# Optimization experiments

Hardware: AMD Instinct MI355X
Metric: run time of the kernel (lower is better)

Reference implementation:

```python
import jax, jax.numpy as jnp
import numpy as np

B, N, DIM, H, DH = 2, 2048, 1024, 16, 64
ALPHA = 32.0 ** 2  # stable_softmax alpha
SCALE = DH ** -0.5


def rotate_half(x):
    # interleaved pairs: (x0, x1, x2, x3, ...) -> (-x1, x0, -x3, x2, ...)
    xp = x.reshape(x.shape[:-1] + (-1, 2))
    return jnp.stack((-xp[..., 1], xp[..., 0]), axis=-1).reshape(x.shape)


def apply_rotary(freqs, t):
    # freqs: [n, d]; t: [b, h, n, d]
    return t * jnp.cos(freqs) + rotate_half(t) * jnp.sin(freqs)


def setup_inputs() -> dict:
    key = jax.random.key(0)
    k0, k1, k2, k3 = jax.random.split(key, 4)
    x = jax.random.normal(k0, (B, N, DIM), jnp.float32)
    rotary_pos_emb = jax.random.normal(k1, (N, DH), jnp.float32)
    w_qkv = jax.random.normal(k2, (DIM, 3 * H * DH), jnp.float32) / np.sqrt(DIM)
    w_out = jax.random.normal(k3, (H * DH, DIM), jnp.float32) / np.sqrt(H * DH)
    b_out = jnp.zeros((DIM,), jnp.float32)
    return {"x": x, "rotary_pos_emb": rotary_pos_emb, "w_qkv": w_qkv,
            "w_out": w_out, "b_out": b_out}


def reference(x, rotary_pos_emb, w_qkv, w_out, b_out):
    b, n, _ = x.shape
    qkv = x @ w_qkv                                  # [b, n, 3*h*d]
    q, k, v = jnp.split(qkv, 3, axis=-1)
    to_heads = lambda t: t.reshape(b, n, H, DH).transpose(0, 2, 1, 3)  # [b,h,n,d]
    q, k, v = map(to_heads, (q, k, v))
    freqs = rotary_pos_emb[:n]
    # source applies rotary emb to q, k AND v
    q = apply_rotary(freqs, q)
    k = apply_rotary(freqs, k)
    v = apply_rotary(freqs, v)
    q = q * SCALE
    dots = jnp.einsum('bhid,bhjd->bhij', q, k)       # [b,h,n,n]
    mask_value = -jnp.finfo(dots.dtype).max
    causal = jnp.triu(jnp.ones((n, n), bool), 1)
    dots = jnp.where(causal, mask_value, dots)
    # stable softmax: divide by alpha, subtract detached max, rescale
    t = dots / ALPHA
    t = t - jax.lax.stop_gradient(jnp.max(t, axis=-1, keepdims=True))
    attn = jax.nn.softmax(t * ALPHA, axis=-1)
    out = jnp.einsum('bhij,bhjd->bhid', attn, v)     # [b,h,n,d]
    out = out.transpose(0, 2, 1, 3).reshape(b, n, H * DH)
    return out @ w_out + b_out
```

## Files before the change

### kernel.cpp

```cpp
#include <hip/hip_runtime.h>
#include <stdint.h>

#define DEV __device__ __forceinline__

typedef __bf16 bf16x8 __attribute__((ext_vector_type(8)));
typedef float  f32x4  __attribute__((ext_vector_type(4)));
typedef short  s16x8  __attribute__((ext_vector_type(8)));

constexpr int Bb   = 2;
constexpr int Nn   = 2048;
constexpr int DIMc = 1024;
constexpr int Hh   = 16;
constexpr int DHc  = 64;
constexpr int BN   = Bb * Nn;
constexpr int QKVC = 3 * Hh * DHc;

DEV ushort f2b(float f) {
  uint32_t u = __float_as_uint(f);
  u += 0x7fffu + ((u >> 16) & 1u);
  return (ushort)(u >> 16);
}

DEV void gload16(const void* g, void* l) {
  __builtin_amdgcn_global_load_lds(
      (const __attribute__((address_space(1))) void*)(uintptr_t)g,
      (__attribute__((address_space(3))) void*)(uint32_t)(uintptr_t)l,
      16, 0, 0);
}

DEV f32x4 mfma16(bf16x8 a, bf16x8 b, f32x4 c) {
  return __builtin_amdgcn_mfma_f32_16x16x32_bf16(a, b, c, 0, 0, 0);
}

DEV uint32_t cvtpk(float lo, float hi) {
  uint32_t r;
  asm("v_cvt_pk_bf16_f32 %0, %1, %2" : "=v"(r) : "v"(lo), "v"(hi));
  return r;
}


__global__ void k_cast_x(const float* __restrict__ x, ushort* __restrict__ xb) {
  int i = blockIdx.x * 256 + threadIdx.x;
  size_t base = (size_t)i * 8;
  s16x8 v;
#pragma unroll
  for (int j = 0; j < 8; ++j) v[j] = (short)f2b(x[base + j]);
  *(s16x8*)(xb + base) = v;
}

__global__ void k_sincos(const float* __restrict__ rope, float2* __restrict__ csT) {
  int i = blockIdx.x * 256 + threadIdx.x;
  float t = rope[i];
  float s, c;
  sincosf(t, &s, &c);
  csT[i] = make_float2(c, s);
}

__global__ void k_transpose_cast(const float* __restrict__ src, ushort* __restrict__ dst,
                                 int K, int Ncols) {
  __shared__ float tile[32][33];
  int nb = blockIdx.x * 32, kb = blockIdx.y * 32;
  int tx = threadIdx.x, ty = threadIdx.y;
#pragma unroll
  for (int i = 0; i < 4; ++i) {
    int k = ty + i * 8;
    tile[k][tx] = src[(size_t)(kb + k) * Ncols + nb + tx];
  }
  __syncthreads();
#pragma unroll
  for (int i = 0; i < 4; ++i) {
    int n = ty + i * 8;
    dst[(size_t)(nb + n) * K + kb + tx] = f2b(tile[tx][n]);
  }
}

DEV void gemm_core(const ushort* __restrict__ A, const ushort* __restrict__ Bt,
                   int rowBase, int colBase, ushort* lA, ushort* lB,
                   f32x4 (&acc)[4][4]) {
  const int tid = threadIdx.x;
  const int lane = tid & 63, w = tid >> 6;
  const int wm = w >> 1, wn = w & 1;
  const int g = lane >> 4, l16 = lane & 15;
  const f32x4 zero = {0.f, 0.f, 0.f, 0.f};
#pragma unroll
  for (int i = 0; i < 4; ++i)
#pragma unroll
    for (int j = 0; j < 4; ++j) acc[i][j] = zero;

  const int c0row = tid >> 2,          c0kc = (tid & 3) ^ ((c0row >> 1) & 3);
  const int c1row = (256 + tid) >> 2,  c1kc = (tid & 3) ^ ((c1row >> 1) & 3);
  const ushort* gA0 = A  + (size_t)(rowBase + c0row) * DIMc + c0kc * 8;
  const ushort* gA1 = A  + (size_t)(rowBase + c1row) * DIMc + c1kc * 8;
  const ushort* gB0 = Bt + (size_t)(colBase + c0row) * DIMc + c0kc * 8;
  const ushort* gB1 = Bt + (size_t)(colBase + c1row) * DIMc + c1kc * 8;
  const size_t o0 = (size_t)(0 * 256 + w * 64) * 8;
  const size_t o1 = (size_t)(1 * 256 + w * 64) * 8;
  constexpr int BUF = 128 * 32;

  gload16(gA0,      lA + o0);        gload16(gB0,      lB + o0);
  gload16(gA1,      lA + o1);        gload16(gB1,      lB + o1);
  gload16(gA0 + 32, lA + BUF + o0);  gload16(gB0 + 32, lB + BUF + o0);
  gload16(gA1 + 32, lA + BUF + o1);  gload16(gB1 + 32, lB + BUF + o1);
  asm volatile("s_waitcnt vmcnt(4)" ::: "memory");
  __builtin_amdgcn_s_barrier();

  int cur = 0;
  for (int k0 = 0; k0 < DIMc; k0 += 32) {
    const ushort* cA = lA + cur * BUF;
    const ushort* cB = lB + cur * BUF;

    bf16x8 af[4], bfr[4];
#pragma unroll
    for (int f = 0; f < 4; ++f) {
      int r  = wm * 64 + f * 16 + l16;
      int r2 = wn * 64 + f * 16 + l16;
      af[f]  = *(const bf16x8*)&cA[r  * 32 + ((g ^ ((r  >> 1) & 3)) << 3)];
      bfr[f] = *(const bf16x8*)&cB[r2 * 32 + ((g ^ ((r2 >> 1) & 3)) << 3)];
    }

    const int kn = k0 + 64;
    if (kn < DIMc) {
      int st = cur + 2; if (st >= 3) st -= 3;
      ushort* nA = lA + st * BUF;
      ushort* nB = lB + st * BUF;
      gload16(gA0 + kn, nA + o0);  gload16(gB0 + kn, nB + o0);
      gload16(gA1 + kn, nA + o1);  gload16(gB1 + kn, nB + o1);
    }

#pragma unroll
    for (int i = 0; i < 4; ++i)
#pragma unroll
      for (int j = 0; j < 4; ++j)
        acc[i][j] = mfma16(af[i], bfr[j], acc[i][j]);

    if (kn < DIMc) {
      asm volatile("s_waitcnt vmcnt(4)" ::: "memory");
    } else if (k0 + 32 < DIMc) {
      asm volatile("s_waitcnt vmcnt(0)" ::: "memory");
    }
    asm volatile("s_waitcnt lgkmcnt(0)" ::: "memory");
    __builtin_amdgcn_s_barrier();
    cur += 1; if (cur == 3) cur = 0;
  }
}

__global__ __launch_bounds__(256) void k_gemm_qkv(
    const ushort* __restrict__ xb, const ushort* __restrict__ wT,
    const float2* __restrict__ csT,
    ushort* __restrict__ Qd, ushort* __restrict__ Kd, ushort* __restrict__ Vd) {
  __shared__ ushort lA[3 * 128 * 32];
  __shared__ ushort lB[3 * 128 * 32];
  f32x4 acc[4][4];
  const int rowBase = blockIdx.y * 128, colBase = blockIdx.x * 128;
  gemm_core(xb, wT, rowBase, colBase, lA, lB, acc);

  const int lane = threadIdx.x & 63, w = threadIdx.x >> 6;
  const int wm = w >> 1, wn = w & 1;
  const int g = lane >> 4, l16 = lane & 15;
#pragma unroll
  for (int fm = 0; fm < 4; ++fm) {
#pragma unroll
    for (int fn = 0; fn < 4; ++fn) {
      int col = colBase + wn * 64 + fn * 16 + l16;
      int sel = col >> 10, hc = col & 1023;
      int h = hc >> 6, d = hc & 63;
      float sgn = (d & 1) ? 1.f : -1.f;
#pragma unroll
      for (int r = 0; r < 4; ++r) {
        float t  = acc[fm][fn][r];
        float tp = __shfl_xor(t, 1);
        int row = rowBase + wm * 64 + fm * 16 + 4 * g + r;
        int b = row >> 11, n = row & 2047;
        float2 cs = csT[n * 64 + d];
        float rv = t * cs.x + sgn * tp * cs.y;
        if (sel == 0) {
          Qd[((size_t)(b * Hh + h) * Nn + n) * DHc + d] = f2b(rv * 0.125f);
        } else if (sel == 1) {
          Kd[((size_t)(b * Hh + h) * Nn + n) * DHc + d] = f2b(rv);
        } else {
          Vd[((size_t)(b * Hh + h) * DHc + d) * Nn + n] = f2b(rv);
        }
      }
    }
  }
}


DEV void stageKV(const ushort* __restrict__ Kh, const ushort* __restrict__ Vh,
                 ushort* lKb, ushort* lVb, int kt, int tid, int w) {
#pragma unroll
  for (int s = 0; s < 2; ++s) {
    int c = s * 256 + tid;
    int row = c >> 3, jst = c & 7;
    int jl = jst ^ (row & 7);
    gload16(Kh + (size_t)(kt * 64 + row) * DHc + jl * 8,
            lKb + (size_t)(s * 256 + w * 64) * 8);
    gload16(Vh + (size_t)row * Nn + kt * 64 + jl * 8,
            lVb + (size_t)(s * 256 + w * 64) * 8);
  }
}

DEV void attn_step(const ushort* lKc, const ushort* lVc, char* lPw,
                   const bf16x8 (&q)[2], f32x4 (&o)[4], float& m, float& l,
                   int kBase, int qg, bool diag, int g, int l16) {
  const f32x4 zero = {0.f, 0.f, 0.f, 0.f};
  f32x4 s[4];
#pragma unroll
  for (int jt = 0; jt < 4; ++jt) s[jt] = zero;

#pragma unroll
  for (int jt = 0; jt < 4; ++jt) {
    int jr = jt * 16 + l16;
#pragma unroll
    for (int d0 = 0; d0 < 2; ++d0) {
      bf16x8 kb = *(const bf16x8*)&lKc[jr * 64 + (((d0 * 4 + g) ^ (jr & 7)) << 3)];
      s[jt] = mfma16(kb, q[d0], s[jt]);
    }
  }

  if (diag) {
#pragma unroll
    for (int jt = 0; jt < 4; ++jt)
#pragma unroll
      for (int r = 0; r < 4; ++r) {
        int j = kBase + jt * 16 + 4 * g + r;
        if (j > qg) s[jt][r] = -3.0e38f;
      }
  }

  float tmax = fmaxf(fmaxf(fmaxf(s[0][0], s[0][1]), fmaxf(s[0][2], s[0][3])),
                     fmaxf(fmaxf(s[1][0], s[1][1]), fmaxf(s[1][2], s[1][3])));
  tmax = fmaxf(tmax, fmaxf(fmaxf(fmaxf(s[2][0], s[2][1]), fmaxf(s[2][2], s[2][3])),
                           fmaxf(fmaxf(s[3][0], s[3][1]), fmaxf(s[3][2], s[3][3]))));
  tmax = fmaxf(tmax, __shfl_xor(tmax, 16));
  tmax = fmaxf(tmax, __shfl_xor(tmax, 32));

  if (!__all(tmax <= m + 8.f)) {
    float mnew = fmaxf(m, tmax);
    float sc = __expf(m - mnew);
#pragma unroll
    for (int dt = 0; dt < 4; ++dt) o[dt] *= sc;
    l *= sc;
    m = mnew;
  }

  float ps = 0.f;
#pragma unroll
  for (int jt = 0; jt < 4; ++jt)
#pragma unroll
    for (int r = 0; r < 4; ++r) {
      float p = __expf(s[jt][r] - m);
      s[jt][r] = p;
      ps += p;
    }
  ps += __shfl_xor(ps, 16);
  ps += __shfl_xor(ps, 32);
  l += ps;

  const int sw = (l16 & 7) << 4;
  char* prow = lPw + l16 * 128;
#pragma unroll
  for (int jt = 0; jt < 4; ++jt) {
    int jo = (jt * 16 + 4 * g) * 2;
    *(uint32_t*)(prow + (jo ^ sw))       = cvtpk(s[jt][0], s[jt][1]);
    *(uint32_t*)(prow + ((jo + 4) ^ sw)) = cvtpk(s[jt][2], s[jt][3]);
  }

  bf16x8 pa[2];
#pragma unroll
  for (int jh = 0; jh < 2; ++jh)
    pa[jh] = *(const bf16x8*)(prow + (((jh * 32 + 8 * g) * 2) ^ sw));
#pragma unroll
  for (int dt = 0; dt < 4; ++dt) {
    int d = dt * 16 + l16;
#pragma unroll
    for (int jh = 0; jh < 2; ++jh) {
      bf16x8 vb = *(const bf16x8*)&lVc[d * 64 + (((jh * 4 + g) ^ (d & 7)) << 3)];
      o[dt] = mfma16(vb, pa[jh], o[dt]);
    }
  }
}

DEV void attn_epi(ushort* __restrict__ ao, int bh, int n, int g,
                  f32x4 (&o)[4], float l) {
  const int b = bh >> 4, h = bh & 15;
  float inv = 1.f / l;
  ushort* dst = ao + (size_t)(b * Nn + n) * (Hh * DHc) + h * 64;
#pragma unroll
  for (int dt = 0; dt < 4; ++dt) {
    uint2 pkd;
    pkd.x = cvtpk(o[dt][0] * inv, o[dt][1] * inv);
    pkd.y = cvtpk(o[dt][2] * inv, o[dt][3] * inv);
    *(uint2*)(dst + dt * 16 + 4 * g) = pkd;
  }
}

__global__ __launch_bounds__(256) void k_attn(
    const ushort* __restrict__ Qd, const ushort* __restrict__ Kd,
    const ushort* __restrict__ Vd, ushort* __restrict__ ao) {
  __shared__ ushort lK[2][64 * 64];
  __shared__ ushort lV[2][64 * 64];
  __shared__ char   lP[4][16 * 128];
  const int tid = threadIdx.x;
  const int lane = tid & 63, w = tid >> 6;
  const int g = lane >> 4, l16 = lane & 15;
  const int bh = blockIdx.y;
  const int p = blockIdx.x;
  const int tA = p, tB = 31 - p;
  const int last = tB;
  const ushort* Qh = Qd + (size_t)bh * Nn * DHc;
  const ushort* Kh = Kd + (size_t)bh * Nn * DHc;
  const ushort* Vh = Vd + (size_t)bh * DHc * Nn;

  const int qgA = tA * 64 + w * 16 + l16;
  const int qgB = tB * 64 + w * 16 + l16;

  bf16x8 qA[2], qB[2];
#pragma unroll
  for (int d0 = 0; d0 < 2; ++d0) {
    qA[d0] = *(const bf16x8*)(Qh + (size_t)qgA * DHc + d0 * 32 + g * 8);
    qB[d0] = *(const bf16x8*)(Qh + (size_t)qgB * DHc + d0 * 32 + g * 8);
  }

  const f32x4 zero = {0.f, 0.f, 0.f, 0.f};
  f32x4 oA[4], oB[4];
#pragma unroll
  for (int dt = 0; dt < 4; ++dt) { oA[dt] = zero; oB[dt] = zero; }
  float mA = -3.0e38f, lA_ = 0.f, mB = -3.0e38f, lB_ = 0.f;

  stageKV(Kh, Vh, lK[0], lV[0], 0, tid, w);

  for (int kt = 0; kt <= last; ++kt) {
    const int cur = kt & 1;
    if (kt < last) {
      stageKV(Kh, Vh, lK[cur ^ 1], lV[cur ^ 1], kt + 1, tid, w);
      asm volatile("s_waitcnt vmcnt(4)" ::: "memory");
    } else {
      asm volatile("s_waitcnt vmcnt(0)" ::: "memory");
    }
    __builtin_amdgcn_s_barrier();

    attn_step(lK[cur], lV[cur], lP[w], qB, oB, mB, lB_, kt * 64, qgB, kt == tB, g, l16);
    if (kt <= tA)
      attn_step(lK[cur], lV[cur], lP[w], qA, oA, mA, lA_, kt * 64, qgA, kt == tA, g, l16);

    __builtin_amdgcn_s_barrier();
  }

  attn_epi(ao, bh, qgA, g, oA, lA_);
  attn_epi(ao, bh, qgB, g, oB, lB_);
}

__global__ __launch_bounds__(256) void k_gemm_out(
    const ushort* __restrict__ ao, const ushort* __restrict__ wT,
    const float* __restrict__ bias, float* __restrict__ out) {
  __shared__ ushort lA[3 * 128 * 32];
  __shared__ ushort lB[3 * 128 * 32];
  f32x4 acc[4][4];
  const int rowBase = blockIdx.y * 128, colBase = blockIdx.x * 128;
  gemm_core(ao, wT, rowBase, colBase, lA, lB, acc);

  const int lane = threadIdx.x & 63, w = threadIdx.x >> 6;
  const int wm = w >> 1, wn = w & 1;
  const int g = lane >> 4, l16 = lane & 15;
#pragma unroll
  for (int fm = 0; fm < 4; ++fm)
#pragma unroll
    for (int fn = 0; fn < 4; ++fn) {
      int col = colBase + wn * 64 + fn * 16 + l16;
#pragma unroll
      for (int r = 0; r < 4; ++r) {
        int row = rowBase + wm * 64 + fm * 16 + 4 * g + r;
        out[(size_t)row * DIMc + col] = acc[fm][fn][r] + bias[col];
      }
    }
}

extern "C" void kernel_launch(void* const* d_in, const int* in_sizes, int n_in,
                              void* d_out, int out_size, void* d_ws, size_t ws_size,
                              hipStream_t stream) {
  const float* x     = (const float*)d_in[0];
  const float* rope  = (const float*)d_in[1];
  const float* w_qkv = (const float*)d_in[2];
  const float* w_out = (const float*)d_in[3];
  const float* b_out = (const float*)d_in[4];
  float* out = (float*)d_out;

  char* ws = (char*)d_ws;
  ushort* xb    = (ushort*)(ws);
  ushort* wqkvT = (ushort*)(ws + 8388608);
  ushort* woutT = (ushort*)(ws + 14680064);
  float2* csT   = (float2*)(ws + 16777216);
  ushort* Qd    = (ushort*)(ws + 17825792);
  ushort* Kd    = (ushort*)(ws + 26214400);
  ushort* Vd    = (ushort*)(ws + 34603008);
  ushort* ao    = (ushort*)(ws + 42991616);

  hipLaunchKernelGGL(k_cast_x, dim3(2048), dim3(256), 0, stream, x, xb);
  hipLaunchKernelGGL(k_transpose_cast, dim3(QKVC / 32, DIMc / 32), dim3(32, 8), 0, stream,
                     w_qkv, wqkvT, DIMc, QKVC);
  hipLaunchKernelGGL(k_transpose_cast, dim3(DIMc / 32, DIMc / 32), dim3(32, 8), 0, stream,
                     w_out, woutT, DIMc, DIMc);
  hipLaunchKernelGGL(k_sincos, dim3(Nn * DHc / 256), dim3(256), 0, stream, rope, csT);
  hipLaunchKernelGGL(k_gemm_qkv, dim3(QKVC / 128, BN / 128), dim3(256), 0, stream,
                     xb, wqkvT, csT, Qd, Kd, Vd);
  hipLaunchKernelGGL(k_attn, dim3(16, Bb * Hh), dim3(256), 0, stream, Qd, Kd, Vd, ao);
  hipLaunchKernelGGL(k_gemm_out, dim3(DIMc / 128, BN / 128), dim3(256), 0, stream,
                     ao, woutT, b_out, out);
}
```

Before: 131.1 us.

## Fuse sincos into cast kernel and shrink out-projection GEMM tile to 64x128

Folds the rotary sin/cos precompute into the x cast kernel, removing one launch. Rewrites the output projection GEMM with its own 64x128 tile loop, a triple-buffered LDS pipeline and four waves each owning a 32-column strip. This doubles the block count from 256 to 512 to fill more CUs on the 4096x1024 output, at the cost of less data reuse per block.

```diff
diff --git a/kernel.cpp b/kernel.cpp
--- a/kernel.cpp
+++ b/kernel.cpp
@@ -39,21 +39,20 @@
 }
 
 
-__global__ void k_cast_x(const float* __restrict__ x, ushort* __restrict__ xb) {
+__global__ void k_cast_x(const float* __restrict__ x, ushort* __restrict__ xb,
+                         const float* __restrict__ rope, float2* __restrict__ csT) {
   int i = blockIdx.x * 256 + threadIdx.x;
   size_t base = (size_t)i * 8;
   s16x8 v;
 #pragma unroll
   for (int j = 0; j < 8; ++j) v[j] = (short)f2b(x[base + j]);
   *(s16x8*)(xb + base) = v;
-}
-
-__global__ void k_sincos(const float* __restrict__ rope, float2* __restrict__ csT) {
-  int i = blockIdx.x * 256 + threadIdx.x;
-  float t = rope[i];
-  float s, c;
-  sincosf(t, &s, &c);
-  csT[i] = make_float2(c, s);
+  if (i < Nn * DHc) {
+    float t = rope[i];
+    float s, c;
+    sincosf(t, &s, &c);
+    csT[i] = make_float2(c, s);
+  }
 }
 
 __global__ void k_transpose_cast(const float* __restrict__ src, ushort* __restrict__ dst,
@@ -354,23 +353,82 @@
 __global__ __launch_bounds__(256) void k_gemm_out(
     const ushort* __restrict__ ao, const ushort* __restrict__ wT,
     const float* __restrict__ bias, float* __restrict__ out) {
-  __shared__ ushort lA[3 * 128 * 32];
+  __shared__ ushort lA[3 * 64 * 32];
   __shared__ ushort lB[3 * 128 * 32];
-  f32x4 acc[4][4];
-  const int rowBase = blockIdx.y * 128, colBase = blockIdx.x * 128;
-  gemm_core(ao, wT, rowBase, colBase, lA, lB, acc);
-
-  const int lane = threadIdx.x & 63, w = threadIdx.x >> 6;
-  const int wm = w >> 1, wn = w & 1;
+  const int tid = threadIdx.x;
+  const int lane = tid & 63, w = tid >> 6;
   const int g = lane >> 4, l16 = lane & 15;
+  const int rowBase = blockIdx.y * 64, colBase = blockIdx.x * 128;
+
+  f32x4 acc[4][2];
+  const f32x4 zero = {0.f, 0.f, 0.f, 0.f};
+#pragma unroll
+  for (int i = 0; i < 4; ++i) { acc[i][0] = zero; acc[i][1] = zero; }
+
+  const int arow = tid >> 2, akc = (tid & 3) ^ ((arow >> 1) & 3);
+  const int b1row = 64 + arow, b1kc = (tid & 3) ^ ((b1row >> 1) & 3);
+  const ushort* gA  = ao + (size_t)(rowBase + arow) * DIMc + akc * 8;
+  const ushort* gB0 = wT + (size_t)(colBase + arow) * DIMc + akc * 8;
+  const ushort* gB1 = wT + (size_t)(colBase + b1row) * DIMc + b1kc * 8;
+  const size_t oA  = (size_t)w * 512;
+  const size_t oB0 = (size_t)w * 512;
+  const size_t oB1 = 2048 + (size_t)w * 512;
+  constexpr int BUFA = 64 * 32, BUFB = 128 * 32;
+
+  gload16(gA,      lA + oA);         gload16(gB0,      lB + oB0);         gload16(gB1,      lB + oB1);
+  gload16(gA + 32, lA + BUFA + oA);  gload16(gB0 + 32, lB + BUFB + oB0);  gload16(gB1 + 32, lB + BUFB + oB1);
+  asm volatile("s_waitcnt vmcnt(3)" ::: "memory");
+  __builtin_amdgcn_s_barrier();
+
+  int cur = 0;
+  for (int k0 = 0; k0 < DIMc; k0 += 32) {
+    const ushort* cA = lA + cur * BUFA;
+    const ushort* cB = lB + cur * BUFB;
+
+    bf16x8 af[4], bfr[2];
+#pragma unroll
+    for (int f = 0; f < 4; ++f) {
+      int r = f * 16 + l16;
+      af[f] = *(const bf16x8*)&cA[r * 32 + ((g ^ ((r >> 1) & 3)) << 3)];
+    }
+#pragma unroll
+    for (int f = 0; f < 2; ++f) {
+      int r2 = w * 32 + f * 16 + l16;
+      bfr[f] = *(const bf16x8*)&cB[r2 * 32 + ((g ^ ((r2 >> 1) & 3)) << 3)];
+    }
+
+    const int kn = k0 + 64;
+    if (kn < DIMc) {
+      int st = cur + 2; if (st >= 3) st -= 3;
+      gload16(gA + kn,  lA + st * BUFA + oA);
+      gload16(gB0 + kn, lB + st * BUFB + oB0);
+      gload16(gB1 + kn, lB + st * BUFB + oB1);
+    }
+
+#pragma unroll
+    for (int i = 0; i < 4; ++i)
+#pragma unroll
+      for (int j = 0; j < 2; ++j)
+        acc[i][j] = mfma16(af[i], bfr[j], acc[i][j]);
+
+    if (kn < DIMc) {
+      asm volatile("s_waitcnt vmcnt(3)" ::: "memory");
+    } else if (k0 + 32 < DIMc) {
+      asm volatile("s_waitcnt vmcnt(0)" ::: "memory");
+    }
+    asm volatile("s_waitcnt lgkmcnt(0)" ::: "memory");
+    __builtin_amdgcn_s_barrier();
+    cur += 1; if (cur == 3) cur = 0;
+  }
+
 #pragma unroll
   for (int fm = 0; fm < 4; ++fm)
 #pragma unroll
-    for (int fn = 0; fn < 4; ++fn) {
-      int col = colBase + wn * 64 + fn * 16 + l16;
+    for (int fn = 0; fn < 2; ++fn) {
+      int col = colBase + w * 32 + fn * 16 + l16;
 #pragma unroll
       for (int r = 0; r < 4; ++r) {
-        int row = rowBase + wm * 64 + fm * 16 + 4 * g + r;
+        int row = rowBase + fm * 16 + 4 * g + r;
         out[(size_t)row * DIMc + col] = acc[fm][fn][r] + bias[col];
       }
     }
@@ -396,15 +454,14 @@
   ushort* Vd    = (ushort*)(ws + 34603008);
   ushort* ao    = (ushort*)(ws + 42991616);
 
-  hipLaunchKernelGGL(k_cast_x, dim3(2048), dim3(256), 0, stream, x, xb);
+  hipLaunchKernelGGL(k_cast_x, dim3(2048), dim3(256), 0, stream, x, xb, rope, csT);
   hipLaunchKernelGGL(k_transpose_cast, dim3(QKVC / 32, DIMc / 32), dim3(32, 8), 0, stream,
                      w_qkv, wqkvT, DIMc, QKVC);
   hipLaunchKernelGGL(k_transpose_cast, dim3(DIMc / 32, DIMc / 32), dim3(32, 8), 0, stream,
                      w_out, woutT, DIMc, DIMc);
-  hipLaunchKernelGGL(k_sincos, dim3(Nn * DHc / 256), dim3(256), 0, stream, rope, csT);
   hipLaunchKernelGGL(k_gemm_qkv, dim3(QKVC / 128, BN / 128), dim3(256), 0, stream,
                      xb, wqkvT, csT, Qd, Kd, Vd);
   hipLaunchKernelGGL(k_attn, dim3(16, Bb * Hh), dim3(256), 0, stream, Qd, Kd, Vd, ao);
-  hipLaunchKernelGGL(k_gemm_out, dim3(DIMc / 128, BN / 128), dim3(256), 0, stream,
+  hipLaunchKernelGGL(k_gemm_out, dim3(DIMc / 128, BN / 64), dim3(256), 0, stream,
                      ao, woutT, b_out, out);
 }
```

After: 130.4 us. No clear change (-0.5%).
